# Performance work log

Hardware: AMD Instinct MI355X
Metric: run time of the kernel (lower is better)

Reference implementation:

```python
import jax, jax.numpy as jnp
import numpy as np

IN_DIMS = 1024
K = 8


def setup_inputs() -> dict:
    key = jax.random.key(0)
    ks = jax.random.split(key, 7)
    s = 1.0 / np.sqrt(IN_DIMS)
    x = jax.random.normal(ks[0], (8, 2048, IN_DIMS), dtype=jnp.float32)
    Wq = jax.random.uniform(ks[1], (IN_DIMS, K), jnp.float32, -s, s)
    bq = jax.random.uniform(ks[2], (K,), jnp.float32, -s, s)
    Wk = jax.random.uniform(ks[3], (IN_DIMS, K), jnp.float32, -s, s)
    bk = jax.random.uniform(ks[4], (K,), jnp.float32, -s, s)
    Wv = jax.random.uniform(ks[5], (IN_DIMS, IN_DIMS), jnp.float32, -s, s)
    bv = jax.random.uniform(ks[6], (IN_DIMS,), jnp.float32, -s, s)
    return {"x": x, "Wq": Wq, "bq": bq, "Wk": Wk, "bk": bk, "Wv": Wv, "bv": bv}


def reference(x, Wq, bq, Wk, bk, Wv, bv):
    # x: [B,S,D]; rank-k projections
    q = jnp.einsum('bsd,dk->bsk', x, Wq) + bq        # [B,S,k]
    k = jnp.einsum('bsd,dk->bsk', x, Wk) + bk        # [B,S,k]
    energy = jnp.einsum('bik,bjk->bij', q, k)        # [B,S,S] (unscaled)
    attention = jax.nn.softmax(energy, axis=-1)
    value = jnp.einsum('bsd,de->bse', x, Wv) + bv    # [B,S,D]
    out = jnp.einsum('bij,bjd->bid', attention, value)
    return (out, attention)
```

## Files before the change

kernel.cpp:

```cpp
#include <hip/hip_runtime.h>


typedef __attribute__((ext_vector_type(8))) __bf16 bf16x8;
typedef __attribute__((ext_vector_type(4))) __bf16 bf16x4;
typedef __attribute__((ext_vector_type(4))) float  f32x4;
typedef unsigned int u32;

#define GLB_CAST(p) ((const __attribute__((address_space(1))) u32*)(p))
#define LDS_CAST(p) ((__attribute__((address_space(3))) u32*)(p))

#define S_BARRIER() { __builtin_amdgcn_s_barrier(); __builtin_amdgcn_sched_barrier(0); }
#define LGKM0()     { asm volatile("s_waitcnt lgkmcnt(0)" ::: "memory"); __builtin_amdgcn_sched_barrier(0); }
#define VMCNT9()    { asm volatile("s_waitcnt vmcnt(9)" ::: "memory"); __builtin_amdgcn_sched_barrier(0); }
#define VMCNT8()    { asm volatile("s_waitcnt vmcnt(8)" ::: "memory"); __builtin_amdgcn_sched_barrier(0); }
#define VMCNT0()    { asm volatile("s_waitcnt vmcnt(0)" ::: "memory"); __builtin_amdgcn_sched_barrier(0); }

static constexpr int    Bn   = 8;
static constexpr int    S    = 2048;
static constexpr int    Dd   = 1024;
static constexpr int    Mtot = Bn * S;
static constexpr size_t OUT0 = (size_t)Bn * S * Dd;

static constexpr size_t OFF_XBF  = 0;
static constexpr size_t OFF_WVT  = OFF_XBF + (size_t)Mtot * Dd * 2;
static constexpr size_t OFF_Q    = OFF_WVT + (size_t)Dd * Dd * 2;
static constexpr size_t OFF_K    = OFF_Q   + (size_t)Mtot * 8 * 4;
static constexpr size_t OFF_VT   = OFF_K   + (size_t)Mtot * 8 * 4;
static constexpr size_t OFF_ATTB = OFF_VT  + (size_t)Bn * Dd * S * 2;
static constexpr size_t WS_NEED  = OFF_ATTB + (size_t)Bn * S * S * 2;

__global__ __launch_bounds__(256) void prep_kernel(
    const float* __restrict__ x, const float* __restrict__ Wq,
    const float* __restrict__ Wk, const float* __restrict__ Wv,
    const float* __restrict__ bq, const float* __restrict__ bk,
    __bf16* __restrict__ xbf, __bf16* __restrict__ wvt,
    float* __restrict__ qb, float* __restrict__ kb)
{
    __shared__ float lt[64][65];
    int bid = blockIdx.x, t = threadIdx.x;
    if (bid < 256) {
        int l = t & 63, w = t >> 6;
        int mbase = (bid * 4 + w) * 16;
        int n = l & 15;
        int dbase = (l >> 4) << 3;
        const float* xr = x + (size_t)(mbase + n) * 1024 + dbase;
        const float* wcol = (n < 8) ? (Wq + n) : (Wk + (n & 7));
        f32x4 acc = {0.f, 0.f, 0.f, 0.f};
        #pragma unroll 4
        for (int kk = 0; kk < 1024; kk += 32) {
            f32x4 a0 = *(const f32x4*)(xr + kk);
            f32x4 a1 = *(const f32x4*)(xr + kk + 4);
            bf16x8 a, b;
            #pragma unroll
            for (int c = 0; c < 4; ++c) { a[c] = (__bf16)a0[c]; a[4 + c] = (__bf16)a1[c]; }
            #pragma unroll
            for (int u = 0; u < 8; ++u) b[u] = (__bf16)wcol[(size_t)(dbase + kk + u) * 8];
            acc = __builtin_amdgcn_mfma_f32_16x16x32_bf16(a, b, acc, 0, 0, 0);
        }
        float bias = (n < 8) ? bq[n] : bk[n & 7];
        #pragma unroll
        for (int r = 0; r < 4; ++r) {
            int m = mbase + ((l >> 4) << 2) + r;
            float v = acc[r] + bias;
            if (n < 8) qb[m * 8 + n] = v;
            else       kb[m * 8 + (n & 7)] = v;
        }
    } else if (bid < 512) {
        int tile = bid - 256;
        int tr = tile >> 4, tc = tile & 15;
        int r0 = t >> 6, c = t & 63;
        #pragma unroll
        for (int i = 0; i < 16; ++i) {
            int row = i * 4 + r0;
            lt[row][c] = Wv[(size_t)(tr * 64 + row) * 1024 + tc * 64 + c];
        }
        __syncthreads();
        #pragma unroll
        for (int i = 0; i < 16; ++i) {
            int er = i * 4 + r0;
            wvt[(size_t)(tc * 64 + er) * 1024 + tr * 64 + c] = (__bf16)lt[c][er];
        }
    } else {
        int bid2 = bid - 512;
        #pragma unroll
        for (int i = 0; i < 4; ++i) {
            size_t idx4 = (size_t)i * 1048576 + (size_t)bid2 * 256 + t;
            f32x4 v = ((const f32x4*)x)[idx4];
            bf16x4 o;
            #pragma unroll
            for (int c = 0; c < 4; ++c) o[c] = (__bf16)v[c];
            ((bf16x4*)xbf)[idx4] = o;
        }
    }
}

__global__ __launch_bounds__(256) void fused_gs_kernel(
    const __bf16* __restrict__ xbf, const __bf16* __restrict__ wvt,
    const float* __restrict__ bv,
    const float* __restrict__ qb, const float* __restrict__ kb,
    __bf16* __restrict__ vtOut, __bf16* __restrict__ attnB)
{
    __shared__ __align__(1024) char smem[32768];
    __shared__ float redm[4], reds[4];
    int bid = blockIdx.x, t = threadIdx.x;
    int seg = bid >> 8;
    int gid = -1, sid = -1;
    if (seg == 0) gid = bid;
    else if (seg == 1) sid = bid - 256;
    else if (seg == 2) gid = bid - 256;
    else if (seg == 3) sid = bid - 512;
    else gid = bid - 512;

    if (sid < 0) {
        int g = ((gid & 7) << 7) | (gid >> 3);
        int mblk = g >> 3, nblk = g & 7;
        int l = t & 63, wid = t >> 6;
        int wmr = wid >> 1, wnc = wid & 1;
        int lr = l & 15, lk = l >> 4;

        int srow = t >> 3;
        int ssl  = (t & 7) ^ (srow & 7);
        const __bf16* gA = xbf + (size_t)(mblk * 128 + srow) * 1024 + ssl * 8;
        const __bf16* gB = wvt + (size_t)(nblk * 128 + srow) * 1024 + ssl * 8;

        int s0 = (lk ^ (lr & 7)) << 3;
        int s1 = ((lk ^ 4) ^ (lr & 7)) << 3;
        int offA0 = (wmr * 64 + lr) * 64 + s0;
        int offA1 = (wmr * 64 + lr) * 64 + s1;
        int offB0 = (wnc * 64 + lr) * 64 + s0;
        int offB1 = (wnc * 64 + lr) * 64 + s1;

        f32x4 acc[4][4] = {};

        for (int tt = 0; tt < 16; ++tt) {
            int kk = tt * 64;
            #pragma unroll
            for (int c = 0; c < 4; ++c) {
                __builtin_amdgcn_global_load_lds(
                    GLB_CAST(gA + (size_t)c * 32 * 1024 + kk),
                    LDS_CAST(smem + c * 4096 + wid * 1024), 16, 0, 0);
                __builtin_amdgcn_global_load_lds(
                    GLB_CAST(gB + (size_t)c * 32 * 1024 + kk),
                    LDS_CAST(smem + 16384 + c * 4096 + wid * 1024), 16, 0, 0);
            }
            __syncthreads();
            const __bf16* As = (const __bf16*)smem;
            const __bf16* Bs = (const __bf16*)(smem + 16384);
            bf16x8 af[4], bfr[4];
            #pragma unroll
            for (int i = 0; i < 4; ++i) af[i]  = *(const bf16x8*)(As + offA0 + i * 1024);
            #pragma unroll
            for (int j = 0; j < 4; ++j) bfr[j] = *(const bf16x8*)(Bs + offB0 + j * 1024);
            #pragma unroll
            for (int i = 0; i < 4; ++i)
                #pragma unroll
                for (int j = 0; j < 4; ++j)
                    acc[i][j] = __builtin_amdgcn_mfma_f32_16x16x32_bf16(af[i], bfr[j], acc[i][j], 0, 0, 0);
            #pragma unroll
            for (int i = 0; i < 4; ++i) af[i]  = *(const bf16x8*)(As + offA1 + i * 1024);
            #pragma unroll
            for (int j = 0; j < 4; ++j) bfr[j] = *(const bf16x8*)(Bs + offB1 + j * 1024);
            #pragma unroll
            for (int i = 0; i < 4; ++i)
                #pragma unroll
                for (int j = 0; j < 4; ++j)
                    acc[i][j] = __builtin_amdgcn_mfma_f32_16x16x32_bf16(af[i], bfr[j], acc[i][j], 0, 0, 0);
            __syncthreads();
        }

        #pragma unroll
        for (int j = 0; j < 4; ++j) {
            int e = (nblk << 7) + wnc * 64 + j * 16 + lr;
            float bias = bv[e];
            #pragma unroll
            for (int i = 0; i < 4; ++i) {
                int m0 = (mblk << 7) + wmr * 64 + i * 16 + (lk << 2);
                int b = m0 >> 11, sA = m0 & 2047;
                bf16x4 o;
                #pragma unroll
                for (int r = 0; r < 4; ++r) o[r] = (__bf16)(acc[i][j][r] + bias);
                *(bf16x4*)&vtOut[(((size_t)(b << 10) + e) << 11) + sA] = o;
            }
        }
    } else {
        int b = sid >> 6, chunk = sid & 63;
        int l = t & 63, w = t >> 6;
        float kr[8][8];
        const float* kbb = kb + ((size_t)b << 14);
        #pragma unroll
        for (int jj = 0; jj < 8; ++jj) {
            f32x4 v0 = *(const f32x4*)(kbb + (size_t)(t * 8 + jj) * 8);
            f32x4 v1 = *(const f32x4*)(kbb + (size_t)(t * 8 + jj) * 8 + 4);
            #pragma unroll
            for (int c = 0; c < 4; ++c) { kr[jj][c] = v0[c]; kr[jj][4 + c] = v1[c]; }
        }
        const float* qrow = qb + ((size_t)b << 14);
        for (int ii = 0; ii < 32; ++ii) {
            int i = (chunk << 5) + ii;
            f32x4 q0 = *(const f32x4*)(qrow + (size_t)i * 8);
            f32x4 q1 = *(const f32x4*)(qrow + (size_t)i * 8 + 4);
            float e[8];
            #pragma unroll
            for (int jj = 0; jj < 8; ++jj) {
                float s = q0[0] * kr[jj][0];
                s = fmaf(q0[1], kr[jj][1], s);
                s = fmaf(q0[2], kr[jj][2], s);
                s = fmaf(q0[3], kr[jj][3], s);
                s = fmaf(q1[0], kr[jj][4], s);
                s = fmaf(q1[1], kr[jj][5], s);
                s = fmaf(q1[2], kr[jj][6], s);
                s = fmaf(q1[3], kr[jj][7], s);
                e[jj] = s;
            }
            float mx = e[0];
            #pragma unroll
            for (int jj = 1; jj < 8; ++jj) mx = fmaxf(mx, e[jj]);
            #pragma unroll
            for (int d = 1; d < 64; d <<= 1) mx = fmaxf(mx, __shfl_xor(mx, d));
            if (l == 0) redm[w] = mx;
            __syncthreads();
            mx = fmaxf(fmaxf(redm[0], redm[1]), fmaxf(redm[2], redm[3]));
            float p[8], sum = 0.f;
            #pragma unroll
            for (int jj = 0; jj < 8; ++jj) { p[jj] = __expf(e[jj] - mx); sum += p[jj]; }
            #pragma unroll
            for (int d = 1; d < 64; d <<= 1) sum += __shfl_xor(sum, d);
            if (l == 0) reds[w] = sum;
            __syncthreads();
            float T = (reds[0] + reds[1]) + (reds[2] + reds[3]);
            float inv = 1.0f / T;
            size_t off = (((size_t)b << 11) + i) * 2048 + (size_t)t * 8;
            bf16x8 ob;
            #pragma unroll
            for (int c = 0; c < 4; ++c) {
                ob[c] = (__bf16)(p[c] * inv); ob[4 + c] = (__bf16)(p[4 + c] * inv);
            }
            *(bf16x8*)(attnB + off) = ob;
        }
    }
}

__device__ __forceinline__ void g1_stageA(const __bf16* Ab, char* smem,
    int slot, int kk, int c, int rowin, int sl8, int wid)
{
    __builtin_amdgcn_global_load_lds(
        GLB_CAST(Ab + (size_t)(c * 64 + rowin) * 2048 + kk + sl8 * 8),
        LDS_CAST(smem + slot * 65536 + c * 8192 + wid * 1024), 16, 0, 0);
}
__device__ __forceinline__ void g1_stageB(const __bf16* Bb, char* smem,
    int slot, int kk, int c, int rowin, int sl8, int wid)
{
    __builtin_amdgcn_global_load_lds(
        GLB_CAST(Bb + (size_t)(c * 64 + rowin) * 2048 + kk + sl8 * 8),
        LDS_CAST(smem + slot * 65536 + 32768 + c * 8192 + wid * 1024), 16, 0, 0);
}

__global__ __launch_bounds__(512, 2) void gemm1_kernel(
    const __bf16* __restrict__ A, const __bf16* __restrict__ Bt,
    float* __restrict__ outF, float* __restrict__ attnF)
{
    constexpr int NT = 32;
    __shared__ __align__(1024) char smem[131072];

    int bid = blockIdx.x;
    int wg = ((bid & 7) << 5) | (bid >> 3);
    int t = threadIdx.x, l = t & 63;
    int wid = t >> 6;
    int wmr = wid >> 2, wnc = wid & 3;

    int bb = wg >> 5; int r = wg & 31;
    int mblk = r >> 2, nblk = r & 3;
    const __bf16* Ab = A + (size_t)bb * S * S + (size_t)mblk * 256 * 2048;
    const __bf16* Bb = Bt + (size_t)bb * Dd * S + (size_t)nblk * 256 * 2048;

    int rowin = t >> 3;
    int sl8 = (t & 7) ^ (rowin & 7);
    int lr = l & 15, lk = l >> 4;

    int crow = nblk * 64 + (t >> 3);
    int ccol = (t & 7) * 8;
    const __bf16* cpSrc = Ab + (size_t)crow * 2048 + ccol;
    float* cpDst = attnF + ((size_t)bb << 22) + ((size_t)(mblk * 256 + crow) << 11) + ccol;
    bf16x8 pv;

    f32x4 acc[8][4] = {};

    #pragma unroll
    for (int c = 0; c < 4; ++c) {
        g1_stageA(Ab, smem, 0, 0, c, rowin, sl8, wid);
        g1_stageB(Bb, smem, 0, 0, c, rowin, sl8, wid);
    }
    #pragma unroll
    for (int c = 0; c < 4; ++c) {
        g1_stageA(Ab, smem, 1, 64, c, rowin, sl8, wid);
        g1_stageB(Bb, smem, 1, 64, c, rowin, sl8, wid);
    }
    VMCNT8();
    S_BARRIER();

    for (int tt = 0; tt < NT; ++tt) {
        int s = tt & 1;
        const __bf16* Asl = (const __bf16*)(smem + s * 65536);
        const __bf16* Bsl = (const __bf16*)(smem + s * 65536 + 32768);
        bool pf = (tt + 2 < NT);
        int kk2 = (tt + 2) * 64;

        if (tt >= 2) {
            f32x4 c0, c1;
            #pragma unroll
            for (int c = 0; c < 4; ++c) { c0[c] = (float)pv[c]; c1[c] = (float)pv[4 + c]; }
            *(f32x4*)(cpDst + (tt - 2) * 64) = c0;
            *(f32x4*)(cpDst + (tt - 2) * 64 + 4) = c1;
        }
        if (tt >= 1) {
            pv = *(const bf16x8*)(cpSrc + (tt - 1) * 64);
        }

        bf16x8 aLo[2][4], aHi[2][4], bLo[2][2], bHi[2][2];

        #pragma unroll
        for (int ks = 0; ks < 2; ++ks) {
            int sa = ks * 4 + lk;
            #pragma unroll
            for (int i = 0; i < 4; ++i) {
                int ra = wmr * 128 + i * 16 + lr;
                aLo[ks][i] = *(const bf16x8*)&Asl[ra * 64 + ((sa ^ (ra & 7)) << 3)];
            }
            #pragma unroll
            for (int j = 0; j < 2; ++j) {
                int rb = wnc * 64 + j * 16 + lr;
                bLo[ks][j] = *(const bf16x8*)&Bsl[rb * 64 + ((sa ^ (rb & 7)) << 3)];
            }
        }
        S_BARRIER(); LGKM0();
        __builtin_amdgcn_s_setprio(1);
        #pragma unroll
        for (int ks = 0; ks < 2; ++ks)
            #pragma unroll
            for (int i = 0; i < 4; ++i)
                #pragma unroll
                for (int j = 0; j < 2; ++j)
                    acc[i][j] = __builtin_amdgcn_mfma_f32_16x16x32_bf16(aLo[ks][i], bLo[ks][j], acc[i][j], 0, 0, 0);
        __builtin_amdgcn_s_setprio(0);
        S_BARRIER();

        #pragma unroll
        for (int ks = 0; ks < 2; ++ks) {
            int sa = ks * 4 + lk;
            #pragma unroll
            for (int j = 0; j < 2; ++j) {
                int rb = wnc * 64 + (j + 2) * 16 + lr;
                bHi[ks][j] = *(const bf16x8*)&Bsl[rb * 64 + ((sa ^ (rb & 7)) << 3)];
            }
        }
        if (pf) {
            g1_stageA(Ab, smem, s, kk2, 0, rowin, sl8, wid);
            g1_stageA(Ab, smem, s, kk2, 2, rowin, sl8, wid);
        }
        S_BARRIER(); LGKM0();
        __builtin_amdgcn_s_setprio(1);
        #pragma unroll
        for (int ks = 0; ks < 2; ++ks)
            #pragma unroll
            for (int i = 0; i < 4; ++i)
                #pragma unroll
                for (int j = 0; j < 2; ++j)
                    acc[i][2 + j] = __builtin_amdgcn_mfma_f32_16x16x32_bf16(aLo[ks][i], bHi[ks][j], acc[i][2 + j], 0, 0, 0);
        __builtin_amdgcn_s_setprio(0);
        S_BARRIER();

        #pragma unroll
        for (int ks = 0; ks < 2; ++ks) {
            int sa = ks * 4 + lk;
            #pragma unroll
            for (int i = 0; i < 4; ++i) {
                int ra = wmr * 128 + (i + 4) * 16 + lr;
                aHi[ks][i] = *(const bf16x8*)&Asl[ra * 64 + ((sa ^ (ra & 7)) << 3)];
            }
        }
        if (pf) {
            #pragma unroll
            for (int c = 0; c < 4; ++c)
                g1_stageB(Bb, smem, s, kk2, c, rowin, sl8, wid);
        }
        S_BARRIER(); LGKM0();
        __builtin_amdgcn_s_setprio(1);
        #pragma unroll
        for (int ks = 0; ks < 2; ++ks)
            #pragma unroll
            for (int i = 0; i < 4; ++i)
                #pragma unroll
                for (int j = 0; j < 2; ++j)
                    acc[4 + i][2 + j] = __builtin_amdgcn_mfma_f32_16x16x32_bf16(aHi[ks][i], bHi[ks][j], acc[4 + i][2 + j], 0, 0, 0);
        __builtin_amdgcn_s_setprio(0);
        S_BARRIER();

        if (pf) {
            g1_stageA(Ab, smem, s, kk2, 1, rowin, sl8, wid);
            g1_stageA(Ab, smem, s, kk2, 3, rowin, sl8, wid);
        }
        S_BARRIER();
        __builtin_amdgcn_s_setprio(1);
        #pragma unroll
        for (int ks = 0; ks < 2; ++ks)
            #pragma unroll
            for (int i = 0; i < 4; ++i)
                #pragma unroll
                for (int j = 0; j < 2; ++j)
                    acc[4 + i][j] = __builtin_amdgcn_mfma_f32_16x16x32_bf16(aHi[ks][i], bLo[ks][j], acc[4 + i][j], 0, 0, 0);
        __builtin_amdgcn_s_setprio(0);

        if (tt == NT - 1) break;
        S_BARRIER();
        if (pf) {
            if (tt == 0) { VMCNT8(); } else { VMCNT9(); }
        } else {
            VMCNT0();
        }
        S_BARRIER();
    }

    {
        f32x4 c0, c1;
        #pragma unroll
        for (int c = 0; c < 4; ++c) { c0[c] = (float)pv[c]; c1[c] = (float)pv[4 + c]; }
        *(f32x4*)(cpDst + (NT - 2) * 64) = c0;
        *(f32x4*)(cpDst + (NT - 2) * 64 + 4) = c1;
        bf16x8 lastv = *(const bf16x8*)(cpSrc + (NT - 1) * 64);
        #pragma unroll
        for (int c = 0; c < 4; ++c) { c0[c] = (float)lastv[c]; c1[c] = (float)lastv[4 + c]; }
        *(f32x4*)(cpDst + (NT - 1) * 64) = c0;
        *(f32x4*)(cpDst + (NT - 1) * 64 + 4) = c1;
    }

    float* ob = outF + (size_t)bb * S * Dd;
    #pragma unroll
    for (int i = 0; i < 8; ++i) {
        int m0 = (mblk << 8) + wmr * 128 + i * 16 + (lk << 2);
        #pragma unroll
        for (int j = 0; j < 4; ++j) {
            int e = (nblk << 8) + wnc * 64 + j * 16 + lr;
            #pragma unroll
            for (int r = 0; r < 4; ++r)
                ob[(size_t)(m0 + r) * 1024 + e] = acc[i][j][r];
        }
    }
}

extern "C" void kernel_launch(void* const* d_in, const int* in_sizes, int n_in,
                              void* d_out, int out_size, void* d_ws, size_t ws_size,
                              hipStream_t stream)
{
    const float* x  = (const float*)d_in[0];
    const float* Wq = (const float*)d_in[1];
    const float* bq = (const float*)d_in[2];
    const float* Wk = (const float*)d_in[3];
    const float* bk = (const float*)d_in[4];
    const float* Wv = (const float*)d_in[5];
    const float* bv = (const float*)d_in[6];

    float* outp  = (float*)d_out;
    float* attnF = outp + OUT0;

    if (ws_size < WS_NEED) return;
    char* ws = (char*)d_ws;
    __bf16* xbf   = (__bf16*)(ws + OFF_XBF);
    __bf16* wvt   = (__bf16*)(ws + OFF_WVT);
    float*  qbuf  = (float*)(ws + OFF_Q);
    float*  kbuf  = (float*)(ws + OFF_K);
    __bf16* vt    = (__bf16*)(ws + OFF_VT);
    __bf16* attnB = (__bf16*)(ws + OFF_ATTB);

    prep_kernel<<<4608, 256, 0, stream>>>(x, Wq, Wk, Wv, bq, bk, xbf, wvt, qbuf, kbuf);
    fused_gs_kernel<<<1536, 256, 0, stream>>>(xbf, wvt, bv, qbuf, kbuf, vt, attnB);
    gemm1_kernel<<<256, 512, 0, stream>>>(attnB, vt, outp, attnF);
}
```

Measured before the change: 189.6 us.

## Replace hand-pipelined 256x256 GEMM with simple 128x128 single-buffered tile kernel

Rewrites the attention-times-value GEMM to use 128x128 output tiles with 256 threads and 1024 blocks instead of 256x256 tiles with 512 threads. The double-buffered, barrier-interleaved prefetch schedule is dropped for a plain load, sync, compute, sync loop over a 32KB LDS buffer. The fp32 copy of the attention matrix is redistributed across the larger grid with 4-element chunks. More, smaller blocks improve occupancy and load balance, but the change gives up load/compute overlap and re-reads the operands more often from global memory.

```diff
diff --git a/kernel.cpp b/kernel.cpp
--- a/kernel.cpp
+++ b/kernel.cpp
@@ -8,12 +8,6 @@
 
 #define GLB_CAST(p) ((const __attribute__((address_space(1))) u32*)(p))
 #define LDS_CAST(p) ((__attribute__((address_space(3))) u32*)(p))
-
-#define S_BARRIER() { __builtin_amdgcn_s_barrier(); __builtin_amdgcn_sched_barrier(0); }
-#define LGKM0()     { asm volatile("s_waitcnt lgkmcnt(0)" ::: "memory"); __builtin_amdgcn_sched_barrier(0); }
-#define VMCNT9()    { asm volatile("s_waitcnt vmcnt(9)" ::: "memory"); __builtin_amdgcn_sched_barrier(0); }
-#define VMCNT8()    { asm volatile("s_waitcnt vmcnt(8)" ::: "memory"); __builtin_amdgcn_sched_barrier(0); }
-#define VMCNT0()    { asm volatile("s_waitcnt vmcnt(0)" ::: "memory"); __builtin_amdgcn_sched_barrier(0); }
 
 static constexpr int    Bn   = 8;
 static constexpr int    S    = 2048;
@@ -240,206 +234,101 @@
     }
 }
 
-__device__ __forceinline__ void g1_stageA(const __bf16* Ab, char* smem,
-    int slot, int kk, int c, int rowin, int sl8, int wid)
-{
-    __builtin_amdgcn_global_load_lds(
-        GLB_CAST(Ab + (size_t)(c * 64 + rowin) * 2048 + kk + sl8 * 8),
-        LDS_CAST(smem + slot * 65536 + c * 8192 + wid * 1024), 16, 0, 0);
-}
-__device__ __forceinline__ void g1_stageB(const __bf16* Bb, char* smem,
-    int slot, int kk, int c, int rowin, int sl8, int wid)
-{
-    __builtin_amdgcn_global_load_lds(
-        GLB_CAST(Bb + (size_t)(c * 64 + rowin) * 2048 + kk + sl8 * 8),
-        LDS_CAST(smem + slot * 65536 + 32768 + c * 8192 + wid * 1024), 16, 0, 0);
-}
-
-__global__ __launch_bounds__(512, 2) void gemm1_kernel(
+__global__ __launch_bounds__(256) void gemm1_kernel(
     const __bf16* __restrict__ A, const __bf16* __restrict__ Bt,
     float* __restrict__ outF, float* __restrict__ attnF)
 {
     constexpr int NT = 32;
-    __shared__ __align__(1024) char smem[131072];
-
-    int bid = blockIdx.x;
-    int wg = ((bid & 7) << 5) | (bid >> 3);
-    int t = threadIdx.x, l = t & 63;
-    int wid = t >> 6;
-    int wmr = wid >> 2, wnc = wid & 3;
-
-    int bb = wg >> 5; int r = wg & 31;
-    int mblk = r >> 2, nblk = r & 3;
-    const __bf16* Ab = A + (size_t)bb * S * S + (size_t)mblk * 256 * 2048;
-    const __bf16* Bb = Bt + (size_t)bb * Dd * S + (size_t)nblk * 256 * 2048;
-
-    int rowin = t >> 3;
-    int sl8 = (t & 7) ^ (rowin & 7);
+    __shared__ __align__(1024) char smem[32768];
+    int bid = blockIdx.x, t = threadIdx.x;
+    int g = ((bid & 7) << 7) | (bid >> 3);
+    int bb = g >> 7;
+    int tile = g & 127;
+    int mblk = tile >> 3, nblk = tile & 7;
+    int l = t & 63, wid = t >> 6;
+    int wmr = wid >> 1, wnc = wid & 1;
     int lr = l & 15, lk = l >> 4;
 
-    int crow = nblk * 64 + (t >> 3);
-    int ccol = (t & 7) * 8;
-    const __bf16* cpSrc = Ab + (size_t)crow * 2048 + ccol;
-    float* cpDst = attnF + ((size_t)bb << 22) + ((size_t)(mblk * 256 + crow) << 11) + ccol;
-    bf16x8 pv;
-
-    f32x4 acc[8][4] = {};
-
-    #pragma unroll
-    for (int c = 0; c < 4; ++c) {
-        g1_stageA(Ab, smem, 0, 0, c, rowin, sl8, wid);
-        g1_stageB(Bb, smem, 0, 0, c, rowin, sl8, wid);
-    }
-    #pragma unroll
-    for (int c = 0; c < 4; ++c) {
-        g1_stageA(Ab, smem, 1, 64, c, rowin, sl8, wid);
-        g1_stageB(Bb, smem, 1, 64, c, rowin, sl8, wid);
-    }
-    VMCNT8();
-    S_BARRIER();
+    const __bf16* Ab = A  + (size_t)bb * S * S  + (size_t)(mblk * 128) * 2048;
+    const __bf16* Bb = Bt + (size_t)bb * Dd * S + (size_t)(nblk * 128) * 2048;
+
+    int srow = t >> 3;
+    int ssl  = (t & 7) ^ (srow & 7);
+    const __bf16* gA = Ab + (size_t)srow * 2048 + ssl * 8;
+    const __bf16* gB = Bb + (size_t)srow * 2048 + ssl * 8;
+
+    int s0 = (lk ^ (lr & 7)) << 3;
+    int s1 = ((lk ^ 4) ^ (lr & 7)) << 3;
+    int offA0 = (wmr * 64 + lr) * 64 + s0;
+    int offA1 = (wmr * 64 + lr) * 64 + s1;
+    int offB0 = (wnc * 64 + lr) * 64 + s0;
+    int offB1 = (wnc * 64 + lr) * 64 + s1;
+
+    int crow = mblk * 128 + nblk * 16 + (t >> 4);
+    int ccol = (t & 15) * 4;
+    const __bf16* cpSrc = A + (size_t)bb * S * S + (size_t)crow * 2048 + ccol;
+    float* cpDst = attnF + ((size_t)bb << 22) + ((size_t)crow << 11) + ccol;
+    bf16x4 pv;
+
+    f32x4 acc[4][4] = {};
 
     for (int tt = 0; tt < NT; ++tt) {
-        int s = tt & 1;
-        const __bf16* Asl = (const __bf16*)(smem + s * 65536);
-        const __bf16* Bsl = (const __bf16*)(smem + s * 65536 + 32768);
-        bool pf = (tt + 2 < NT);
-        int kk2 = (tt + 2) * 64;
-
-        if (tt >= 2) {
-            f32x4 c0, c1;
-            #pragma unroll
-            for (int c = 0; c < 4; ++c) { c0[c] = (float)pv[c]; c1[c] = (float)pv[4 + c]; }
-            *(f32x4*)(cpDst + (tt - 2) * 64) = c0;
-            *(f32x4*)(cpDst + (tt - 2) * 64 + 4) = c1;
+        int kk = tt * 64;
+        #pragma unroll
+        for (int c = 0; c < 4; ++c) {
+            __builtin_amdgcn_global_load_lds(
+                GLB_CAST(gA + (size_t)c * 32 * 2048 + kk),
+                LDS_CAST(smem + c * 4096 + wid * 1024), 16, 0, 0);
+            __builtin_amdgcn_global_load_lds(
+                GLB_CAST(gB + (size_t)c * 32 * 2048 + kk),
+                LDS_CAST(smem + 16384 + c * 4096 + wid * 1024), 16, 0, 0);
         }
         if (tt >= 1) {
-            pv = *(const bf16x8*)(cpSrc + (tt - 1) * 64);
-        }
-
-        bf16x8 aLo[2][4], aHi[2][4], bLo[2][2], bHi[2][2];
-
-        #pragma unroll
-        for (int ks = 0; ks < 2; ++ks) {
-            int sa = ks * 4 + lk;
-            #pragma unroll
-            for (int i = 0; i < 4; ++i) {
-                int ra = wmr * 128 + i * 16 + lr;
-                aLo[ks][i] = *(const bf16x8*)&Asl[ra * 64 + ((sa ^ (ra & 7)) << 3)];
-            }
-            #pragma unroll
-            for (int j = 0; j < 2; ++j) {
-                int rb = wnc * 64 + j * 16 + lr;
-                bLo[ks][j] = *(const bf16x8*)&Bsl[rb * 64 + ((sa ^ (rb & 7)) << 3)];
-            }
-        }
-        S_BARRIER(); LGKM0();
-        __builtin_amdgcn_s_setprio(1);
-        #pragma unroll
-        for (int ks = 0; ks < 2; ++ks)
-            #pragma unroll
-            for (int i = 0; i < 4; ++i)
-                #pragma unroll
-                for (int j = 0; j < 2; ++j)
-                    acc[i][j] = __builtin_amdgcn_mfma_f32_16x16x32_bf16(aLo[ks][i], bLo[ks][j], acc[i][j], 0, 0, 0);
-        __builtin_amdgcn_s_setprio(0);
-        S_BARRIER();
-
-        #pragma unroll
-        for (int ks = 0; ks < 2; ++ks) {
-            int sa = ks * 4 + lk;
-            #pragma unroll
-            for (int j = 0; j < 2; ++j) {
-                int rb = wnc * 64 + (j + 2) * 16 + lr;
-                bHi[ks][j] = *(const bf16x8*)&Bsl[rb * 64 + ((sa ^ (rb & 7)) << 3)];
-            }
-        }
-        if (pf) {
-            g1_stageA(Ab, smem, s, kk2, 0, rowin, sl8, wid);
-            g1_stageA(Ab, smem, s, kk2, 2, rowin, sl8, wid);
-        }
-        S_BARRIER(); LGKM0();
-        __builtin_amdgcn_s_setprio(1);
-        #pragma unroll
-        for (int ks = 0; ks < 2; ++ks)
-            #pragma unroll
-            for (int i = 0; i < 4; ++i)
-                #pragma unroll
-                for (int j = 0; j < 2; ++j)
-                    acc[i][2 + j] = __builtin_amdgcn_mfma_f32_16x16x32_bf16(aLo[ks][i], bHi[ks][j], acc[i][2 + j], 0, 0, 0);
-        __builtin_amdgcn_s_setprio(0);
-        S_BARRIER();
-
-        #pragma unroll
-        for (int ks = 0; ks < 2; ++ks) {
-            int sa = ks * 4 + lk;
-            #pragma unroll
-            for (int i = 0; i < 4; ++i) {
-                int ra = wmr * 128 + (i + 4) * 16 + lr;
-                aHi[ks][i] = *(const bf16x8*)&Asl[ra * 64 + ((sa ^ (ra & 7)) << 3)];
-            }
-        }
-        if (pf) {
-            #pragma unroll
-            for (int c = 0; c < 4; ++c)
-                g1_stageB(Bb, smem, s, kk2, c, rowin, sl8, wid);
-        }
-        S_BARRIER(); LGKM0();
-        __builtin_amdgcn_s_setprio(1);
-        #pragma unroll
-        for (int ks = 0; ks < 2; ++ks)
-            #pragma unroll
-            for (int i = 0; i < 4; ++i)
-                #pragma unroll
-                for (int j = 0; j < 2; ++j)
-                    acc[4 + i][2 + j] = __builtin_amdgcn_mfma_f32_16x16x32_bf16(aHi[ks][i], bHi[ks][j], acc[4 + i][2 + j], 0, 0, 0);
-        __builtin_amdgcn_s_setprio(0);
-        S_BARRIER();
-
-        if (pf) {
-            g1_stageA(Ab, smem, s, kk2, 1, rowin, sl8, wid);
-            g1_stageA(Ab, smem, s, kk2, 3, rowin, sl8, wid);
-        }
-        S_BARRIER();
-        __builtin_amdgcn_s_setprio(1);
-        #pragma unroll
-        for (int ks = 0; ks < 2; ++ks)
-            #pragma unroll
-            for (int i = 0; i < 4; ++i)
-                #pragma unroll
-                for (int j = 0; j < 2; ++j)
-                    acc[4 + i][j] = __builtin_amdgcn_mfma_f32_16x16x32_bf16(aHi[ks][i], bLo[ks][j], acc[4 + i][j], 0, 0, 0);
-        __builtin_amdgcn_s_setprio(0);
-
-        if (tt == NT - 1) break;
-        S_BARRIER();
-        if (pf) {
-            if (tt == 0) { VMCNT8(); } else { VMCNT9(); }
-        } else {
-            VMCNT0();
-        }
-        S_BARRIER();
+            f32x4 cv;
+            #pragma unroll
+            for (int c = 0; c < 4; ++c) cv[c] = (float)pv[c];
+            *(f32x4*)(cpDst + (tt - 1) * 64) = cv;
+        }
+        pv = *(const bf16x4*)(cpSrc + tt * 64);
+        __syncthreads();
+        const __bf16* As = (const __bf16*)smem;
+        const __bf16* Bs = (const __bf16*)(smem + 16384);
+        bf16x8 af[4], bfr[4];
+        #pragma unroll
+        for (int i = 0; i < 4; ++i) af[i]  = *(const bf16x8*)(As + offA0 + i * 1024);
+        #pragma unroll
+        for (int j = 0; j < 4; ++j) bfr[j] = *(const bf16x8*)(Bs + offB0 + j * 1024);
+        #pragma unroll
+        for (int i = 0; i < 4; ++i)
+            #pragma unroll
+            for (int j = 0; j < 4; ++j)
+                acc[i][j] = __builtin_amdgcn_mfma_f32_16x16x32_bf16(af[i], bfr[j], acc[i][j], 0, 0, 0);
+        #pragma unroll
+        for (int i = 0; i < 4; ++i) af[i]  = *(const bf16x8*)(As + offA1 + i * 1024);
+        #pragma unroll
+        for (int j = 0; j < 4; ++j) bfr[j] = *(const bf16x8*)(Bs + offB1 + j * 1024);
+        #pragma unroll
+        for (int i = 0; i < 4; ++i)
+            #pragma unroll
+            for (int j = 0; j < 4; ++j)
+                acc[i][j] = __builtin_amdgcn_mfma_f32_16x16x32_bf16(af[i], bfr[j], acc[i][j], 0, 0, 0);
+        __syncthreads();
     }
 
     {
-        f32x4 c0, c1;
-        #pragma unroll
-        for (int c = 0; c < 4; ++c) { c0[c] = (float)pv[c]; c1[c] = (float)pv[4 + c]; }
-        *(f32x4*)(cpDst + (NT - 2) * 64) = c0;
-        *(f32x4*)(cpDst + (NT - 2) * 64 + 4) = c1;
-        bf16x8 lastv = *(const bf16x8*)(cpSrc + (NT - 1) * 64);
-        #pragma unroll
-        for (int c = 0; c < 4; ++c) { c0[c] = (float)lastv[c]; c1[c] = (float)lastv[4 + c]; }
-        *(f32x4*)(cpDst + (NT - 1) * 64) = c0;
-        *(f32x4*)(cpDst + (NT - 1) * 64 + 4) = c1;
+        f32x4 cv;
+        #pragma unroll
+        for (int c = 0; c < 4; ++c) cv[c] = (float)pv[c];
+        *(f32x4*)(cpDst + (NT - 1) * 64) = cv;
     }
 
     float* ob = outF + (size_t)bb * S * Dd;
     #pragma unroll
-    for (int i = 0; i < 8; ++i) {
-        int m0 = (mblk << 8) + wmr * 128 + i * 16 + (lk << 2);
+    for (int i = 0; i < 4; ++i) {
+        int m0 = (mblk << 7) + wmr * 64 + i * 16 + (lk << 2);
         #pragma unroll
         for (int j = 0; j < 4; ++j) {
-            int e = (nblk << 8) + wnc * 64 + j * 16 + lr;
+            int e = (nblk << 7) + wnc * 64 + j * 16 + lr;
             #pragma unroll
             for (int r = 0; r < 4; ++r)
                 ob[(size_t)(m0 + r) * 1024 + e] = acc[i][j][r];
@@ -473,5 +362,5 @@
 
     prep_kernel<<<4608, 256, 0, stream>>>(x, Wq, Wk, Wv, bq, bk, xbf, wvt, qbuf, kbuf);
     fused_gs_kernel<<<1536, 256, 0, stream>>>(xbf, wvt, bv, qbuf, kbuf, vt, attnB);
-    gemm1_kernel<<<256, 512, 0, stream>>>(attnB, vt, outp, attnF);
+    gemm1_kernel<<<1024, 256, 0, stream>>>(attnB, vt, outp, attnF);
 }
```

After: 217.7 us. +14.8%, slower.
